# Kernel optimization log

Hardware: AMD Instinct MI355X
Metric: run time of the kernel (lower is better)

Reference implementation:

```python
import jax, jax.numpy as jnp
import numpy as np

E = 1024
H = 16
D = E // H
FF = 4 * E
EPS = 1e-5


def _layernorm(x, g, b):
    mu = jnp.mean(x, axis=-1, keepdims=True)
    var = jnp.mean(jnp.square(x - mu), axis=-1, keepdims=True)
    return (x - mu) * jax.lax.rsqrt(var + EPS) * g + b


def setup_inputs() -> dict:
    key = jax.random.key(0)
    ks = jax.random.split(key, 8)
    s_e = 1.0 / np.sqrt(E)
    s_f = 1.0 / np.sqrt(FF)
    return {
        "x": jax.random.normal(ks[0], (2, 2048, E), dtype=jnp.float32),
        "ln1_g": jnp.ones((E,), jnp.float32),
        "ln1_b": jnp.zeros((E,), jnp.float32),
        "qkv_w": jax.random.normal(ks[1], (E, 3 * E), jnp.float32) * s_e,
        "qkv_b": jnp.zeros((3 * E,), jnp.float32),
        "proj_w": jax.random.normal(ks[2], (E, E), jnp.float32) * s_e,
        "proj_b": jnp.zeros((E,), jnp.float32),
        "ln2_g": jnp.ones((E,), jnp.float32),
        "ln2_b": jnp.zeros((E,), jnp.float32),
        "fc1_w": jax.random.normal(ks[3], (E, FF), jnp.float32) * s_e,
        "fc1_b": jnp.zeros((FF,), jnp.float32),
        "fc2_w": jax.random.normal(ks[4], (FF, E), jnp.float32) * s_f,
        "fc2_b": jnp.zeros((E,), jnp.float32),
    }


def reference(x, ln1_g, ln1_b, qkv_w, qkv_b, proj_w, proj_b,
              ln2_g, ln2_b, fc1_w, fc1_b, fc2_w, fc2_b):
    B, N, _ = x.shape
    # --- pre-norm MHA ---
    h = _layernorm(x, ln1_g, ln1_b)
    qkv = (h @ qkv_w + qkv_b).reshape(B, N, 3, H, D)
    q, k, v = [jnp.moveaxis(qkv[:, :, i], 2, 1) for i in range(3)]  # [B,H,N,D]
    scores = jnp.einsum('bhnd,bhmd->bhnm', q, k) / np.sqrt(D)
    attn = jax.nn.softmax(scores, axis=-1)
    out = jnp.einsum('bhnm,bhmd->bnhd', attn, v).reshape(B, N, E)
    x = x + out @ proj_w + proj_b
    # --- pre-norm MLP ---
    h = _layernorm(x, ln2_g, ln2_b)
    h = jax.nn.gelu(h @ fc1_w + fc1_b, approximate=False)
    x = x + h @ fc2_w + fc2_b
    return x
```

## Files before the change

### kernel.cpp

```cpp
#include <hip/hip_runtime.h>
#include <math.h>

#define E_DIM 1024
#define NHEAD 16
#define HDIM 64
#define FF_DIM 4096
#define NBATCH 2
#define SEQLEN 2048
#define NTOK 4096
#define LN_EPS 1e-5f

typedef unsigned short bfu;
typedef __attribute__((ext_vector_type(8))) short bf16x8;
typedef __attribute__((ext_vector_type(4))) float f32x4;

static __device__ __forceinline__ bfu f2bf(float f) {
  unsigned u = __float_as_uint(f);
  return (bfu)((u + 0x7fffu + ((u >> 16) & 1u)) >> 16);
}

static __device__ __forceinline__ void gld16(const bfu* g, bfu* l) {
  __builtin_amdgcn_global_load_lds(
      (const __attribute__((address_space(1))) void*)g,
      (__attribute__((address_space(3))) void*)l, 16, 0, 0);
}

__global__ __launch_bounds__(256) void transpose_cvt(
    const float* __restrict__ W, bfu* __restrict__ Wt, int R, int C) {
  __shared__ float t[32][33];
  int c0 = blockIdx.x * 32, r0 = blockIdx.y * 32;
#pragma unroll
  for (int i = 0; i < 32; i += 8)
    t[threadIdx.y + i][threadIdx.x] =
        W[(size_t)(r0 + threadIdx.y + i) * C + c0 + threadIdx.x];
  __syncthreads();
#pragma unroll
  for (int i = 0; i < 32; i += 8)
    Wt[(size_t)(c0 + threadIdx.y + i) * R + r0 + threadIdx.x] =
        f2bf(t[threadIdx.x][threadIdx.y + i]);
}

__global__ __launch_bounds__(256) void ln_kernel(
    const float* __restrict__ x, const float* __restrict__ g,
    const float* __restrict__ b, bfu* __restrict__ out) {
  int row = blockIdx.x;
  float4 v = reinterpret_cast<const float4*>(x + (size_t)row * E_DIM)[threadIdx.x];
  float s = v.x + v.y + v.z + v.w;
  float s2 = v.x * v.x + v.y * v.y + v.z * v.z + v.w * v.w;
#pragma unroll
  for (int off = 1; off < 64; off <<= 1) {
    s += __shfl_xor(s, off);
    s2 += __shfl_xor(s2, off);
  }
  __shared__ float red[8];
  int wv = threadIdx.x >> 6;
  if ((threadIdx.x & 63) == 0) { red[wv] = s; red[4 + wv] = s2; }
  __syncthreads();
  s = red[0] + red[1] + red[2] + red[3];
  s2 = red[4] + red[5] + red[6] + red[7];
  float mu = s * (1.f / E_DIM);
  float var = s2 * (1.f / E_DIM) - mu * mu;
  float rs = rsqrtf(var + LN_EPS);
  int c = threadIdx.x * 4;
  ushort4 o;
  o.x = f2bf((v.x - mu) * rs * g[c + 0] + b[c + 0]);
  o.y = f2bf((v.y - mu) * rs * g[c + 1] + b[c + 1]);
  o.z = f2bf((v.z - mu) * rs * g[c + 2] + b[c + 2]);
  o.w = f2bf((v.w - mu) * rs * g[c + 3] + b[c + 3]);
  reinterpret_cast<ushort4*>(out + (size_t)row * E_DIM)[threadIdx.x] = o;
}

template <int EP, int BN>
__global__ __launch_bounds__(256) void gemm_kernel(
    const bfu* __restrict__ A, const bfu* __restrict__ Bt,
    int M, int N, int K,
    const float* __restrict__ bias, const float* __restrict__ resid,
    float* __restrict__ outf, bfu* __restrict__ outb,
    bfu* __restrict__ qo, bfu* __restrict__ ko, bfu* __restrict__ vo) {
  constexpr int NJ = BN / 32;
  __shared__ __align__(16) bfu As[128][64];
  __shared__ __align__(16) bfu Bs[BN][64];
  const int tid = threadIdx.x;
  const int lane = tid & 63, wv = tid >> 6;
  const int wr = (wv >> 1) * 64, wc = (wv & 1) * (BN / 2);
  const int gx = gridDim.x, nwg = gx * gridDim.y;
  const int hw = blockIdx.y * gx + blockIdx.x;
  const int lg = (hw & 7) * (nwg >> 3) + (hw >> 3);
  const int m0 = (lg / gx) * 128, n0 = (lg % gx) * BN;

  f32x4 acc[4][NJ];
#pragma unroll
  for (int i = 0; i < 4; i++)
#pragma unroll
    for (int j = 0; j < NJ; j++) acc[i][j] = (f32x4){0.f, 0.f, 0.f, 0.f};

  const int sr = lane >> 3, sc = (lane & 7) * 8;
  for (int k0 = 0; k0 < K; k0 += 64) {
#pragma unroll
    for (int c = 0; c < 4; c++) {
      int r = wv * 32 + c * 8;
      gld16(A + (size_t)(m0 + r + sr) * K + k0 + sc, &As[r][0]);
    }
#pragma unroll
    for (int c = 0; c < BN / 32; c++) {
      int r = wv * (BN / 4) + c * 8;
      gld16(Bt + (size_t)(n0 + r + sr) * K + k0 + sc, &Bs[r][0]);
    }
    __syncthreads();
#pragma unroll
    for (int kk = 0; kk < 2; kk++) {
      const int krd = kk * 32 + (lane >> 4) * 8;
      bf16x8 af[4], bfr[NJ];
#pragma unroll
      for (int i = 0; i < 4; i++)
        af[i] = *reinterpret_cast<const bf16x8*>(&As[wr + i * 16 + (lane & 15)][krd]);
#pragma unroll
      for (int j = 0; j < NJ; j++)
        bfr[j] = *reinterpret_cast<const bf16x8*>(&Bs[wc + j * 16 + (lane & 15)][krd]);
#pragma unroll
      for (int i = 0; i < 4; i++)
#pragma unroll
        for (int j = 0; j < NJ; j++)
          acc[i][j] = __builtin_amdgcn_mfma_f32_16x16x32_bf16(af[i], bfr[j], acc[i][j], 0, 0, 0);
    }
    __syncthreads();
  }

  const int cr = (lane >> 4) * 4, cc = lane & 15;
#pragma unroll
  for (int i = 0; i < 4; i++) {
#pragma unroll
    for (int j = 0; j < NJ; j++) {
      const int gn = n0 + wc + j * 16 + cc;
      const float bb = bias[gn];
#pragma unroll
      for (int r = 0; r < 4; r++) {
        const int gm = m0 + wr + i * 16 + cr + r;
        float val = acc[i][j][r] + bb;
        if (EP == 0) {
          int which = gn >> 10, rem = gn & 1023;
          int hh = rem >> 6, dd = rem & 63;
          int b_ = gm >> 11, nn = gm & 2047;
          size_t dst = (((size_t)(b_ * NHEAD + hh)) * SEQLEN + nn) * HDIM + dd;
          if (which == 0) qo[dst] = f2bf(val * 0.125f);
          else if (which == 1) ko[dst] = f2bf(val);
          else vo[dst] = f2bf(val);
        } else if (EP == 1) {
          outf[(size_t)gm * N + gn] = val + resid[(size_t)gm * N + gn];
        } else if (EP == 2) {
          outb[(size_t)gm * N + gn] = f2bf(0.5f * val * (1.f + erff(val * 0.70710678f)));
        } else {
          outf[(size_t)gm * N + gn] = val + resid[(size_t)gm * N + gn];
        }
      }
    }
  }
}

__global__ __launch_bounds__(256) void attn_kernel(
    const bfu* __restrict__ q, const bfu* __restrict__ kbuf,
    const bfu* __restrict__ vbuf, bfu* __restrict__ o) {
  __shared__ __align__(16) bfu Ks[64][64];
  __shared__ __align__(16) bfu Vt[64][72];
  __shared__ __align__(16) bfu Ps[4][16][72];

  const int hw = blockIdx.y * gridDim.x + blockIdx.x;
  const int lg = (hw & 7) * 128 + (hw >> 3);
  const int bh = lg >> 5;
  const int q0 = (lg & 31) * 64;
  const int tid = threadIdx.x, lane = tid & 63, wv = tid >> 6;
  const size_t base = (size_t)bh * SEQLEN * HDIM;
  const bfu* qp = q + base;
  const bfu* kp = kbuf + base;
  const bfu* vp = vbuf + base;

  const int qr = q0 + wv * 16 + (lane & 15);
  bf16x8 qf[2];
  qf[0] = *reinterpret_cast<const bf16x8*>(qp + (size_t)qr * HDIM + (lane >> 4) * 8);
  qf[1] = *reinterpret_cast<const bf16x8*>(qp + (size_t)qr * HDIM + 32 + (lane >> 4) * 8);

  float mrun = -1e30f, lrun = 0.f;
  f32x4 oacc[4];
#pragma unroll
  for (int d = 0; d < 4; d++) oacc[d] = (f32x4){0.f, 0.f, 0.f, 0.f};

  const int sr = lane >> 3;
  const int scs = ((lane & 7) ^ (sr & 7)) * 8;
  const int vrow = tid & 63, vcb = (tid >> 6) * 16;

  for (int kt = 0; kt < SEQLEN; kt += 64) {
#pragma unroll
    for (int c = 0; c < 2; c++) {
      int ch = wv * 2 + c;
      gld16(kp + (size_t)(kt + ch * 8 + sr) * HDIM + scs, &Ks[ch * 8][0]);
    }
    bf16x8 v0 = *reinterpret_cast<const bf16x8*>(vp + (size_t)(kt + vrow) * HDIM + vcb);
    bf16x8 v1 = *reinterpret_cast<const bf16x8*>(vp + (size_t)(kt + vrow) * HDIM + vcb + 8);
#pragma unroll
    for (int j = 0; j < 8; j++) {
      Vt[vcb + j][vrow] = (bfu)(unsigned short)v0[j];
      Vt[vcb + 8 + j][vrow] = (bfu)(unsigned short)v1[j];
    }
    __syncthreads();

    f32x4 st[4];
    __builtin_amdgcn_s_setprio(1);
#pragma unroll
    for (int kc = 0; kc < 4; kc++) {
      f32x4 a = (f32x4){0.f, 0.f, 0.f, 0.f};
#pragma unroll
      for (int kk = 0; kk < 2; kk++) {
        int ce = (kk * 32 + (lane >> 4) * 8) ^ ((lane & 7) << 3);
        bf16x8 kf = *reinterpret_cast<const bf16x8*>(&Ks[kc * 16 + (lane & 15)][ce]);
        a = __builtin_amdgcn_mfma_f32_16x16x32_bf16(kf, qf[kk], a, 0, 0, 0);
      }
      st[kc] = a;
    }
    __builtin_amdgcn_s_setprio(0);

    float t0 = fmaxf(fmaxf(st[0][0], st[0][1]), fmaxf(st[0][2], st[0][3]));
    float t1 = fmaxf(fmaxf(st[1][0], st[1][1]), fmaxf(st[1][2], st[1][3]));
    float t2 = fmaxf(fmaxf(st[2][0], st[2][1]), fmaxf(st[2][2], st[2][3]));
    float t3 = fmaxf(fmaxf(st[3][0], st[3][1]), fmaxf(st[3][2], st[3][3]));
    float t = fmaxf(fmaxf(t0, t1), fmaxf(t2, t3));
    t = fmaxf(t, __shfl_xor(t, 16));
    t = fmaxf(t, __shfl_xor(t, 32));

    bool resc = t > mrun + 8.f;
    if (__any(resc)) {
      float alpha = resc ? __expf(mrun - t) : 1.f;
      if (resc) mrun = t;
      lrun *= alpha;
#pragma unroll
      for (int r = 0; r < 4; r++) {
        float ar = __shfl(alpha, (lane >> 4) * 4 + r);
#pragma unroll
        for (int d = 0; d < 4; d++) oacc[d][r] *= ar;
      }
    }

    float p[4][4], ps = 0.f;
#pragma unroll
    for (int kc = 0; kc < 4; kc++)
#pragma unroll
      for (int r = 0; r < 4; r++) {
        p[kc][r] = __expf(st[kc][r] - mrun);
        ps += p[kc][r];
      }
    ps += __shfl_xor(ps, 16);
    ps += __shfl_xor(ps, 32);
    lrun += ps;

    const int qcol = lane & 15, g4 = (lane >> 4) * 4;
#pragma unroll
    for (int kc = 0; kc < 4; kc++) {
      ushort4 pk;
      pk.x = f2bf(p[kc][0]); pk.y = f2bf(p[kc][1]);
      pk.z = f2bf(p[kc][2]); pk.w = f2bf(p[kc][3]);
      *reinterpret_cast<ushort4*>(&Ps[wv][qcol][kc * 16 + g4]) = pk;
    }

    bf16x8 pf[2];
#pragma unroll
    for (int ks = 0; ks < 2; ks++)
      pf[ks] = *reinterpret_cast<const bf16x8*>(
          &Ps[wv][lane & 15][ks * 32 + (lane >> 4) * 8]);
    __builtin_amdgcn_s_setprio(1);
#pragma unroll
    for (int d = 0; d < 4; d++) {
#pragma unroll
      for (int ks = 0; ks < 2; ks++) {
        bf16x8 vf = *reinterpret_cast<const bf16x8*>(
            &Vt[d * 16 + (lane & 15)][ks * 32 + (lane >> 4) * 8]);
        oacc[d] = __builtin_amdgcn_mfma_f32_16x16x32_bf16(pf[ks], vf, oacc[d], 0, 0, 0);
      }
    }
    __builtin_amdgcn_s_setprio(0);
    __syncthreads();
  }

  int b_ = bh >> 4, hh = bh & 15;
#pragma unroll
  for (int r = 0; r < 4; r++) {
    float lr = __shfl(lrun, (lane >> 4) * 4 + r);
    float rl = 1.f / lr;
#pragma unroll
    for (int d = 0; d < 4; d++) {
      int row = q0 + wv * 16 + (lane >> 4) * 4 + r;
      int col = hh * HDIM + d * 16 + (lane & 15);
      o[((size_t)(b_ * SEQLEN + row)) * E_DIM + col] = f2bf(oacc[d][r] * rl);
    }
  }
}

extern "C" void kernel_launch(void* const* d_in, const int* in_sizes, int n_in,
                              void* d_out, int out_size, void* d_ws, size_t ws_size,
                              hipStream_t stream) {
  (void)in_sizes; (void)n_in; (void)out_size; (void)ws_size;
  const float* x      = (const float*)d_in[0];
  const float* ln1_g  = (const float*)d_in[1];
  const float* ln1_b  = (const float*)d_in[2];
  const float* qkv_w  = (const float*)d_in[3];
  const float* qkv_b  = (const float*)d_in[4];
  const float* proj_w = (const float*)d_in[5];
  const float* proj_b = (const float*)d_in[6];
  const float* ln2_g  = (const float*)d_in[7];
  const float* ln2_b  = (const float*)d_in[8];
  const float* fc1_w  = (const float*)d_in[9];
  const float* fc1_b  = (const float*)d_in[10];
  const float* fc2_w  = (const float*)d_in[11];
  const float* fc2_b  = (const float*)d_in[12];
  float* out = (float*)d_out;

  char* p = (char*)d_ws;
  auto carve = [&](size_t n) { char* r = p; p += (n + 255) & ~(size_t)255; return r; };
  bfu* qkv_wt  = (bfu*)carve((size_t)3 * E_DIM * E_DIM * 2);
  bfu* proj_wt = (bfu*)carve((size_t)E_DIM * E_DIM * 2);
  bfu* fc1_wt  = (bfu*)carve((size_t)FF_DIM * E_DIM * 2);
  bfu* fc2_wt  = (bfu*)carve((size_t)E_DIM * FF_DIM * 2);
  bfu* hbuf    = (bfu*)carve((size_t)NTOK * E_DIM * 2);
  bfu* region  = (bfu*)carve((size_t)NTOK * FF_DIM * 2);
  float* x1    = (float*)carve((size_t)NTOK * E_DIM * 4);
  bfu* qb = region;
  bfu* kb = region + (size_t)NTOK * E_DIM;
  bfu* vb = region + (size_t)2 * NTOK * E_DIM;
  bfu* ao = region + (size_t)3 * NTOK * E_DIM;
  bfu* h3 = region;

  dim3 tb(32, 8);
  transpose_cvt<<<dim3(3 * E_DIM / 32, E_DIM / 32), tb, 0, stream>>>(qkv_w, qkv_wt, E_DIM, 3 * E_DIM);
  transpose_cvt<<<dim3(E_DIM / 32, E_DIM / 32), tb, 0, stream>>>(proj_w, proj_wt, E_DIM, E_DIM);
  transpose_cvt<<<dim3(FF_DIM / 32, E_DIM / 32), tb, 0, stream>>>(fc1_w, fc1_wt, E_DIM, FF_DIM);
  transpose_cvt<<<dim3(E_DIM / 32, FF_DIM / 32), tb, 0, stream>>>(fc2_w, fc2_wt, FF_DIM, E_DIM);

  ln_kernel<<<NTOK, 256, 0, stream>>>(x, ln1_g, ln1_b, hbuf);
  gemm_kernel<0, 128><<<dim3(3 * E_DIM / 128, NTOK / 128), 256, 0, stream>>>(
      hbuf, qkv_wt, NTOK, 3 * E_DIM, E_DIM, qkv_b, nullptr, nullptr, nullptr, qb, kb, vb);
  attn_kernel<<<dim3(SEQLEN / 64, NBATCH * NHEAD), 256, 0, stream>>>(qb, kb, vb, ao);
  gemm_kernel<1, 64><<<dim3(E_DIM / 64, NTOK / 128), 256, 0, stream>>>(
      ao, proj_wt, NTOK, E_DIM, E_DIM, proj_b, x, x1, nullptr, nullptr, nullptr, nullptr);
  ln_kernel<<<NTOK, 256, 0, stream>>>(x1, ln2_g, ln2_b, hbuf);
  gemm_kernel<2, 128><<<dim3(FF_DIM / 128, NTOK / 128), 256, 0, stream>>>(
      hbuf, fc1_wt, NTOK, FF_DIM, E_DIM, fc1_b, nullptr, nullptr, h3, nullptr, nullptr, nullptr);
  gemm_kernel<3, 64><<<dim3(E_DIM / 64, NTOK / 128), 256, 0, stream>>>(
      h3, fc2_wt, NTOK, E_DIM, FF_DIM, fc2_b, x1, out, nullptr, nullptr, nullptr, nullptr);
}
```

Baseline: 442.5 us.

## Double-buffer GEMM LDS tiles and XOR-swizzle columns to avoid bank conflicts

The GEMM main loop now uses two LDS buffers, so the global-to-LDS load of the next K tile is issued before computing on the current tile, overlapping memory latency with MFMA work. Global source columns are XOR-swizzled by row and read back with a matching swizzle, meant to spread the fragment reads across LDS banks. The bf16 conversion helper also switches to the library intrinsic. This doubles LDS use per block, which may cut occupancy, and correctness depends on the load-to-sync ordering of the async LDS loads.

```diff
diff --git a/kernel.cpp b/kernel.cpp
--- a/kernel.cpp
+++ b/kernel.cpp
@@ -1,4 +1,5 @@
 #include <hip/hip_runtime.h>
+#include <hip/hip_bf16.h>
 #include <math.h>
 
 #define E_DIM 1024
@@ -15,8 +16,8 @@
 typedef __attribute__((ext_vector_type(4))) float f32x4;
 
 static __device__ __forceinline__ bfu f2bf(float f) {
-  unsigned u = __float_as_uint(f);
-  return (bfu)((u + 0x7fffu + ((u >> 16) & 1u)) >> 16);
+  __hip_bfloat16 h = __float2bfloat16(f);
+  return *reinterpret_cast<bfu*>(&h);
 }
 
 static __device__ __forceinline__ void gld16(const bfu* g, bfu* l) {
@@ -78,8 +79,8 @@
     float* __restrict__ outf, bfu* __restrict__ outb,
     bfu* __restrict__ qo, bfu* __restrict__ ko, bfu* __restrict__ vo) {
   constexpr int NJ = BN / 32;
-  __shared__ __align__(16) bfu As[128][64];
-  __shared__ __align__(16) bfu Bs[BN][64];
+  __shared__ __align__(16) bfu As[2][128][64];
+  __shared__ __align__(16) bfu Bs[2][BN][64];
   const int tid = threadIdx.x;
   const int lane = tid & 63, wv = tid >> 6;
   const int wr = (wv >> 1) * 64, wc = (wv & 1) * (BN / 2);
@@ -94,29 +95,39 @@
 #pragma unroll
     for (int j = 0; j < NJ; j++) acc[i][j] = (f32x4){0.f, 0.f, 0.f, 0.f};
 
-  const int sr = lane >> 3, sc = (lane & 7) * 8;
-  for (int k0 = 0; k0 < K; k0 += 64) {
+  const int sr = lane >> 3;
+  const int scs = ((lane & 7) ^ (sr & 7)) * 8;
+  const int rsw = (lane & 7) << 3;
+
+  auto stage = [&](int buf, int k0) {
 #pragma unroll
     for (int c = 0; c < 4; c++) {
       int r = wv * 32 + c * 8;
-      gld16(A + (size_t)(m0 + r + sr) * K + k0 + sc, &As[r][0]);
+      gld16(A + (size_t)(m0 + r + sr) * K + k0 + scs, &As[buf][r][0]);
     }
 #pragma unroll
     for (int c = 0; c < BN / 32; c++) {
       int r = wv * (BN / 4) + c * 8;
-      gld16(Bt + (size_t)(n0 + r + sr) * K + k0 + sc, &Bs[r][0]);
-    }
-    __syncthreads();
+      gld16(Bt + (size_t)(n0 + r + sr) * K + k0 + scs, &Bs[buf][r][0]);
+    }
+  };
+
+  stage(0, 0);
+  __syncthreads();
+  const int NT = K >> 6;
+  int cur = 0;
+  for (int t = 0; t < NT; t++) {
+    if (t + 1 < NT) stage(cur ^ 1, (t + 1) * 64);
 #pragma unroll
     for (int kk = 0; kk < 2; kk++) {
-      const int krd = kk * 32 + (lane >> 4) * 8;
+      const int ce = (kk * 32 + (lane >> 4) * 8) ^ rsw;
       bf16x8 af[4], bfr[NJ];
 #pragma unroll
       for (int i = 0; i < 4; i++)
-        af[i] = *reinterpret_cast<const bf16x8*>(&As[wr + i * 16 + (lane & 15)][krd]);
+        af[i] = *reinterpret_cast<const bf16x8*>(&As[cur][wr + i * 16 + (lane & 15)][ce]);
 #pragma unroll
       for (int j = 0; j < NJ; j++)
-        bfr[j] = *reinterpret_cast<const bf16x8*>(&Bs[wc + j * 16 + (lane & 15)][krd]);
+        bfr[j] = *reinterpret_cast<const bf16x8*>(&Bs[cur][wc + j * 16 + (lane & 15)][ce]);
 #pragma unroll
       for (int i = 0; i < 4; i++)
 #pragma unroll
@@ -124,6 +135,7 @@
           acc[i][j] = __builtin_amdgcn_mfma_f32_16x16x32_bf16(af[i], bfr[j], acc[i][j], 0, 0, 0);
     }
     __syncthreads();
+    cur ^= 1;
   }
 
   const int cr = (lane >> 4) * 4, cc = lane & 15;
```

Result: faster. 359.7 us (-18.7%).
